# Kernel tuning notes

Measured on AMD Instinct MI355X. Metric: run time of the kernel, lower is better.

Reference implementation:

```python
import jax, jax.numpy as jnp
import numpy as np

B, C_IN, IMG = 4, 1, 256
E, P = 800, 4            # embed_size, patch_size
H, DH, M = 8, 64, 64     # heads, dim_head=heads**2, num_landmarks
N = (IMG // P) ** 2      # 4096 tokens
OUT = 256                # output_size
RESK = 33                # lucidrains residual depthwise conv kernel
BN_EPS = 1e-5
LN_EPS = 1e-5
PINV_ITERS = 6


def setup_inputs() -> dict:
    key = jax.random.key(0)
    ks = iter(jax.random.split(key, 32))
    def nrm(shape, s=0.02):
        return jax.random.normal(next(ks), shape, jnp.float32) * s
    inp = {"x": jax.random.normal(next(ks), (B, C_IN, IMG, IMG), jnp.float32)}
    # conv stack: (in, out, kernel); last conv has stride=P, padding=0
    for i, (ci, co, kk) in enumerate([(C_IN, 64, 3), (64, 128, 3), (128, 256, 3), (256, E, P)]):
        inp[f"w{i}"] = nrm((co, ci, kk, kk), 0.05)
        inp[f"b{i}"] = jnp.zeros((co,), jnp.float32)
        inp[f"g{i}"] = jnp.ones((co,), jnp.float32)    # BN gamma
        inp[f"be{i}"] = jnp.zeros((co,), jnp.float32)  # BN beta
        inp[f"mu{i}"] = nrm((co,), 0.1)                # BN running mean
        inp[f"var{i}"] = jax.random.uniform(next(ks), (co,), jnp.float32, 0.5, 1.5)
    inp["qkv_w"] = nrm((E, 3 * H * DH))      # to_qkv (no bias)
    inp["out_w"] = nrm((H * DH, E))          # to_out linear
    inp["out_b"] = jnp.zeros((E,), jnp.float32)
    inp["res_w"] = nrm((H, 1, RESK, 1), 0.05)  # depthwise residual conv over token dim
    inp["ln_g"] = jnp.ones((E,), jnp.float32)
    inp["ln_b"] = jnp.zeros((E,), jnp.float32)
    inp["head_w"] = nrm((E, OUT * OUT // N))   # Linear(800, 16)
    inp["head_b"] = jnp.zeros((OUT * OUT // N,), jnp.float32)
    return inp


def conv2d(x, w, b, stride, pad):
    y = jax.lax.conv_general_dilated(x, w, (stride, stride), [(pad, pad), (pad, pad)],
                                     dimension_numbers=("NCHW", "OIHW", "NCHW"))
    return y + b[None, :, None, None]


def bn(x, g, be, mu, var):
    s = g * jax.lax.rsqrt(var + BN_EPS)  # eval-mode BatchNorm
    return x * s[None, :, None, None] + (be - mu * s)[None, :, None, None]


def moore_penrose_pinv(a, iters=PINV_ITERS):
    I = jnp.eye(a.shape[-1], dtype=a.dtype)
    z = jnp.swapaxes(a, -1, -2) / (jnp.max(jnp.abs(a).sum(-1)) * jnp.max(jnp.abs(a).sum(-2)))
    for _ in range(iters):
        az = a @ z
        z = 0.25 * z @ (13.0 * I - az @ (15.0 * I - az @ (7.0 * I - az)))
    return z


def reference(x, w0, b0, g0, be0, mu0, var0, w1, b1, g1, be1, mu1, var1,
              w2, b2, g2, be2, mu2, var2, w3, b3, g3, be3, mu3, var3,
              qkv_w, out_w, out_b, res_w, ln_g, ln_b, head_w, head_b):
    # ---- PatchEmbedConv ----
    h = x
    blocks = [(w0, b0, g0, be0, mu0, var0, 1, 1), (w1, b1, g1, be1, mu1, var1, 1, 1),
              (w2, b2, g2, be2, mu2, var2, 1, 1), (w3, b3, g3, be3, mu3, var3, P, 0)]
    for w, b, g, be, mu, var, st, pd in blocks:
        h = jax.nn.relu(bn(conv2d(h, w, b, st, pd), g, be, mu, var))
    tok = h.reshape(B, E, N).transpose(0, 2, 1)  # [B, N, E]

    # ---- NystromAttention (n % m == 0, so no front padding needed) ----
    qkv = tok @ qkv_w  # [B, N, 3*H*DH]
    q, k, v = [t.reshape(B, N, H, DH).transpose(0, 2, 1, 3) for t in jnp.split(qkv, 3, axis=-1)]
    q = q * (DH ** -0.5)
    l = N // M
    q_l = q.reshape(B, H, M, l, DH).mean(3)  # landmark means over consecutive blocks
    k_l = k.reshape(B, H, M, l, DH).mean(3)
    a1 = jax.nn.softmax(jnp.einsum("bhnd,bhmd->bhnm", q, k_l), axis=-1)    # [B,H,N,M]
    a2 = jax.nn.softmax(jnp.einsum("bhmd,bhkd->bhmk", q_l, k_l), axis=-1)  # [B,H,M,M]
    a3 = jax.nn.softmax(jnp.einsum("bhmd,bhnd->bhmn", q_l, k), axis=-1)    # [B,H,M,N]
    out = (a1 @ moore_penrose_pinv(a2)) @ (a3 @ v)  # [B,H,N,DH]
    # residual depthwise conv over the token dim of v (groups = heads)
    res = jax.lax.conv_general_dilated(v, res_w, (1, 1), [(RESK // 2, RESK // 2), (0, 0)],
                                       dimension_numbers=("NCHW", "OIHW", "NCHW"),
                                       feature_group_count=H)
    out = out + res
    out = out.transpose(0, 2, 1, 3).reshape(B, N, H * DH)
    out = out @ out_w + out_b  # [B, N, E]

    # ---- LayerNorm ----
    mu_t = out.mean(-1, keepdims=True)
    var_t = out.var(-1, keepdims=True)
    out = (out - mu_t) * jax.lax.rsqrt(var_t + LN_EPS) * ln_g + ln_b

    # ---- reconstruction head ----
    y = jax.nn.sigmoid(out @ head_w + head_b)  # [B, N, OUT*OUT/N]
    return y.reshape(-1, 1, OUT, OUT)
```

## Files before the change

### kernel.cpp

```cpp
#include <hip/hip_runtime.h>

#define DI __device__ __forceinline__

constexpr float BN_EPS_C = 1e-5f;
constexpr float LN_EPS_C = 1e-5f;

typedef _Float16 half8 __attribute__((ext_vector_type(8)));
typedef float f32x4 __attribute__((ext_vector_type(4)));

constexpr size_t B_H0   = 0;
constexpr size_t B_H1   = 8388608;
constexpr size_t B_H2   = 25165824;
constexpr size_t B_Q    = 25165824;
constexpr size_t B_V    = 58720256;
constexpr size_t B_KT   = 75497472;
constexpr size_t B_ATT  = 92274688;
constexpr size_t B_LNB  = 25165824;
constexpr size_t B_TOK  = 159383552;
constexpr size_t B_WP1  = 185597952;
constexpr size_t B_WP2  = 185745408;
constexpr size_t B_WP3  = 186335232;
constexpr size_t B_QKVT = 192888832;
constexpr size_t B_OWT  = 195346432;
constexpr size_t B_QL   = 196165632;
constexpr size_t B_KL   = 196689920;
constexpr size_t B_KLH  = 197214208;
constexpr size_t B_A2   = 197476352;
constexpr size_t B_W2T  = 198524928;
constexpr size_t B_A3V  = 198787072;
constexpr size_t B_SCAL = 199311360;
constexpr size_t B_HWH  = 199311424;

DI void gl_lds16(const _Float16* g, _Float16* l) {
  __builtin_amdgcn_global_load_lds(
      (const __attribute__((address_space(1))) void*)g,
      (__attribute__((address_space(3))) void*)l, 16, 0, 0);
}

template <int LP, int RP>
DI void mm16v(const float* L, const float* R, int r0, int c0, float reg[4][4]) {
  #pragma unroll
  for (int i = 0; i < 4; ++i)
    #pragma unroll
    for (int j = 0; j < 4; ++j) reg[i][j] = 0.f;
  #pragma unroll 4
  for (int dd = 0; dd < 64; dd += 4) {
    f32x4 l[4], rv[4];
    #pragma unroll
    for (int i = 0; i < 4; ++i)
      l[i] = *reinterpret_cast<const f32x4*>(&L[(size_t)(r0 + i) * LP + dd]);
    #pragma unroll
    for (int u = 0; u < 4; ++u)
      rv[u] = *reinterpret_cast<const f32x4*>(&R[(size_t)(dd + u) * RP + c0]);
    #pragma unroll
    for (int i = 0; i < 4; ++i)
      #pragma unroll
      for (int u = 0; u < 4; ++u)
        #pragma unroll
        for (int j = 0; j < 4; ++j)
          reg[i][j] = fmaf(l[i][u], rv[u][j], reg[i][j]);
  }
}

__global__ void k_pack_all(
    const float* __restrict__ w1, const float* __restrict__ w2c, const float* __restrict__ w3,
    const float* __restrict__ qkvw, const float* __restrict__ outw, const float* __restrict__ headw,
    _Float16* __restrict__ wp1, _Float16* __restrict__ wp2, _Float16* __restrict__ wp3,
    _Float16* __restrict__ qkvT, _Float16* __restrict__ owT, _Float16* __restrict__ hwh,
    float* __restrict__ scal) {
  size_t i = (size_t)blockIdx.x * 256 + threadIdx.x;
  if (i < 73728) {
    int q = i % 9, ci = (i / 9) % 64, co = i / (9 * 64);
    wp1[((size_t)co * 9 + q) * 64 + ci] = (_Float16)w1[i];
  } else if (i < 368640) {
    size_t j = i - 73728;
    int q = j % 9, ci = (j / 9) % 128, co = j / (9 * 128);
    wp2[((size_t)co * 9 + q) * 128 + ci] = (_Float16)w2c[j];
  } else if (i < 3645440) {
    size_t j = i - 368640;
    int q = j % 16, ci = (j / 16) % 256, co = j / (16 * 256);
    wp3[((size_t)co * 16 + q) * 256 + ci] = (_Float16)w3[j];
  } else if (i < 4874240) {
    size_t j = i - 3645440;
    int n = j % 1536, k = j / 1536;
    qkvT[(size_t)n * 800 + k] = (_Float16)qkvw[j];
  } else if (i < 5283840) {
    size_t j = i - 4874240;
    int n = j % 800, k = j / 800;
    owT[(size_t)n * 512 + k] = (_Float16)outw[j];
  } else if (i < 5296640) {
    size_t j = i - 5283840;
    int n = j % 16, k = j / 16;
    hwh[(size_t)n * 800 + k] = (_Float16)headw[j];
  } else if (i < 5296642) {
    scal[i - 5296640] = 0.f;
  }
}

__global__ __launch_bounds__(256) void k_conv0(
    const float* __restrict__ xb, const float* __restrict__ w0, const float* __restrict__ b0,
    const float* __restrict__ g0, const float* __restrict__ be0, const float* __restrict__ mu0,
    const float* __restrict__ var0, _Float16* __restrict__ h0) {
  const int t = threadIdx.x, co = t & 63, xg = t >> 6;
  const int y = blockIdx.x;
  const int x0 = blockIdx.y * 64 + xg * 16;
  float wreg[9];
  #pragma unroll
  for (int q = 0; q < 9; ++q) wreg[q] = w0[co * 9 + q];
  float s = g0[co] * rsqrtf(var0[co] + BN_EPS_C);
  float sh = fmaf(b0[co] - mu0[co], s, be0[co]);
  #pragma unroll 4
  for (int xl = 0; xl < 16; ++xl) {
    int xx = x0 + xl;
    float acc = 0.f;
    #pragma unroll
    for (int dy = 0; dy < 3; ++dy) {
      int yy = y + dy - 1;
      if ((unsigned)yy >= 256u) continue;
      #pragma unroll
      for (int dx = 0; dx < 3; ++dx) {
        int xi = xx + dx - 1;
        if ((unsigned)xi >= 256u) continue;
        acc = fmaf(wreg[dy * 3 + dx], xb[yy * 256 + xi], acc);
      }
    }
    float v = fmaxf(fmaf(acc, s, sh), 0.f);
    h0[((size_t)y * 256 + xx) * 64 + co] = (_Float16)v;
  }
}

template <int CI>
__global__ __launch_bounds__(256) void k_convs(
    const _Float16* __restrict__ in, const _Float16* __restrict__ wp,
    const float* __restrict__ bias, const float* __restrict__ g, const float* __restrict__ be,
    const float* __restrict__ mu, const float* __restrict__ var,
    _Float16* __restrict__ out, int CO, int NCT) {
  __shared__ _Float16 Ab[2][128 * 40];
  __shared__ _Float16 Bb[2][128 * 40];
  constexpr int CPQ = CI / 32;
  constexpr int NCK = 9 * CPQ;
  const int t = threadIdx.x;
  const int bid = blockIdx.x;
  const int xcd = bid & 7, slot = bid >> 3;
  const int pj = slot / NCT, cc = slot % NCT;
  const int p = pj * 8 + xcd;
  const int r0 = p * 128, c0 = cc * 128;

  const int ma = t >> 2, kga = t & 3;
  int ry[2], rx[2];
  #pragma unroll
  for (int s = 0; s < 2; ++s) {
    int r = r0 + ma + s * 64;
    ry[s] = r >> 8;
    rx[s] = r & 255;
  }
  const _Float16* baseB[2];
  #pragma unroll
  for (int s = 0; s < 2; ++s)
    baseB[s] = wp + (size_t)(c0 + ma + s * 64) * 9 * CI + kga * 8;
  const int wo = ma * 40 + kga * 8;

  auto loadA = [&](int s, int ck) -> half8 {
    int q = ck / CPQ, coff = (ck % CPQ) * 32;
    int yy = ry[s] + q / 3 - 1;
    int xx = rx[s] + q % 3 - 1;
    half8 a = {};
    if ((unsigned)yy < 256u && (unsigned)xx < 256u)
      a = *reinterpret_cast<const half8*>(in + ((size_t)yy * 256 + xx) * CI + coff + kga * 8);
    return a;
  };

  {
    half8 a0 = loadA(0, 0), a1 = loadA(1, 0);
    half8 b0v = *reinterpret_cast<const half8*>(baseB[0]);
    half8 b1v = *reinterpret_cast<const half8*>(baseB[1]);
    *reinterpret_cast<half8*>(&Ab[0][wo]) = a0;
    *reinterpret_cast<half8*>(&Ab[0][wo + 2560]) = a1;
    *reinterpret_cast<half8*>(&Bb[0][wo]) = b0v;
    *reinterpret_cast<half8*>(&Bb[0][wo + 2560]) = b1v;
  }
  __syncthreads();

  const int w = t >> 6, lo = t & 15, hi = (t >> 4) & 3;
  const int wm = w >> 1, wn = w & 1;
  const int roA = (wm * 64 + lo) * 40 + 8 * hi;
  const int roB = (wn * 64 + lo) * 40 + 8 * hi;
  f32x4 acc[4][4] = {};

  for (int ck = 0; ck < NCK; ++ck) {
    const int cur = ck & 1;
    const bool more = (ck + 1 < NCK);
    half8 rA0, rA1, rB0, rB1;
    if (more) {
      rA0 = loadA(0, ck + 1);
      rA1 = loadA(1, ck + 1);
      rB0 = *reinterpret_cast<const half8*>(baseB[0] + (ck + 1) * 32);
      rB1 = *reinterpret_cast<const half8*>(baseB[1] + (ck + 1) * 32);
    }
    half8 af[4], bf[4];
    #pragma unroll
    for (int mi = 0; mi < 4; ++mi)
      af[mi] = *reinterpret_cast<const half8*>(&Ab[cur][roA + mi * 640]);
    #pragma unroll
    for (int ni = 0; ni < 4; ++ni)
      bf[ni] = *reinterpret_cast<const half8*>(&Bb[cur][roB + ni * 640]);
    #pragma unroll
    for (int mi = 0; mi < 4; ++mi)
      #pragma unroll
      for (int ni = 0; ni < 4; ++ni)
        acc[mi][ni] = __builtin_amdgcn_mfma_f32_16x16x32_f16(af[mi], bf[ni], acc[mi][ni], 0, 0, 0);
    if (more) {
      *reinterpret_cast<half8*>(&Ab[cur ^ 1][wo]) = rA0;
      *reinterpret_cast<half8*>(&Ab[cur ^ 1][wo + 2560]) = rA1;
      *reinterpret_cast<half8*>(&Bb[cur ^ 1][wo]) = rB0;
      *reinterpret_cast<half8*>(&Bb[cur ^ 1][wo + 2560]) = rB1;
    }
    __syncthreads();
  }

  #pragma unroll
  for (int ni = 0; ni < 4; ++ni) {
    int co = c0 + wn * 64 + ni * 16 + lo;
    float s = g[co] * rsqrtf(var[co] + BN_EPS_C);
    float sh = fmaf(bias[co] - mu[co], s, be[co]);
    #pragma unroll
    for (int mi = 0; mi < 4; ++mi)
      #pragma unroll
      for (int rr = 0; rr < 4; ++rr) {
        int row = r0 + wm * 64 + mi * 16 + hi * 4 + rr;
        float v = fmaxf(fmaf(acc[mi][ni][rr], s, sh), 0.f);
        out[(size_t)row * CO + co] = (_Float16)v;
      }
  }
}

__global__ __launch_bounds__(256) void k_c3(
    const _Float16* __restrict__ h2, const _Float16* __restrict__ wp3,
    const float* __restrict__ b3, const float* __restrict__ g3, const float* __restrict__ be3,
    const float* __restrict__ mu3, const float* __restrict__ var3,
    _Float16* __restrict__ tok) {
  __shared__ _Float16 Abuf[2][128 * 32];
  __shared__ _Float16 Bbuf[2][160 * 32];
  const int t = threadIdx.x;
  const int bid = blockIdx.x;
  const int xcd = bid & 7, slot = bid >> 3;
  const int pj = slot / 5, cc = slot % 5;
  const int p = pj * 8 + xcd;
  const int r0 = p * 128, c0 = cc * 160;
  const int img = r0 >> 12;
  const _Float16* h2i = h2 + (size_t)img * 16777216;

  const int w = t >> 6, l = t & 63;
  const int kslot = (l & 3) ^ ((l >> 3) & 3);
  const _Float16* gA[2];
  #pragma unroll
  for (int s = 0; s < 2; ++s) {
    int mar = 16 * w + (l >> 2) + 64 * s;
    int r = r0 + mar;
    int py = (r & 4095) >> 6, px = r & 63;
    gA[s] = h2i + ((size_t)py * 1024 + px * 4) * 256 + kslot * 8;
  }
  const _Float16* gB[3];
  #pragma unroll
  for (int s = 0; s < 3; ++s) {
    int rb = 16 * w + (l >> 2) + 64 * s;
    if (rb > 159) rb = 159;
    gB[s] = wp3 + (size_t)(c0 + rb) * 4096 + kslot * 8;
  }

  const int lo = t & 15, hi = (t >> 4) & 3;
  const int wm = w >> 1, wn = w & 1;
  const int sl = hi ^ ((lo >> 1) & 3);
  const int roA = (wm * 64 + lo) * 32 + sl * 8;
  const int roB = (wn * 80 + lo) * 32 + sl * 8;

  f32x4 acc[4][5] = {};

  auto STAGE = [&](int buf, int ck) {
    const int kn = ck << 5;
    const int q = kn >> 8;
    const size_t aoff = (size_t)(q >> 2) * 65536 + (size_t)(q & 3) * 256 + (kn & 255);
    _Float16* Ad = &Abuf[buf][512 * w];
    _Float16* Bd = &Bbuf[buf][512 * w];
    gl_lds16(gA[0] + aoff, Ad);
    gl_lds16(gA[1] + aoff, Ad + 2048);
    gl_lds16(gB[0] + kn, Bd);
    gl_lds16(gB[1] + kn, Bd + 2048);
    if (w < 2) gl_lds16(gB[2] + kn, Bd + 4096);
  };

  STAGE(0, 0);
  __syncthreads();

  for (int ck = 0; ck < 128; ++ck) {
    const int cur = ck & 1;
    if (ck + 1 < 128) STAGE(cur ^ 1, ck + 1);
    half8 af[4], bf[5];
    #pragma unroll
    for (int mi = 0; mi < 4; ++mi)
      af[mi] = *reinterpret_cast<const half8*>(&Abuf[cur][roA + mi * 512]);
    #pragma unroll
    for (int ni = 0; ni < 5; ++ni)
      bf[ni] = *reinterpret_cast<const half8*>(&Bbuf[cur][roB + ni * 512]);
    #pragma unroll
    for (int mi = 0; mi < 4; ++mi)
      #pragma unroll
      for (int ni = 0; ni < 5; ++ni)
        acc[mi][ni] = __builtin_amdgcn_mfma_f32_16x16x32_f16(af[mi], bf[ni], acc[mi][ni], 0, 0, 0);
    __syncthreads();
  }

  #pragma unroll
  for (int ni = 0; ni < 5; ++ni) {
    int col = c0 + wn * 80 + ni * 16 + lo;
    float s = g3[col] * rsqrtf(var3[col] + BN_EPS_C);
    float sh = fmaf(b3[col] - mu3[col], s, be3[col]);
    #pragma unroll
    for (int mi = 0; mi < 4; ++mi)
      #pragma unroll
      for (int rr = 0; rr < 4; ++rr) {
        int row = r0 + wm * 64 + mi * 16 + hi * 4 + rr;
        float v = fmaxf(fmaf(acc[mi][ni][rr], s, sh), 0.f);
        tok[(size_t)row * 800 + col] = (_Float16)v;
      }
  }
}

__global__ __launch_bounds__(256) void k_qkv_s(
    const _Float16* __restrict__ tok, const _Float16* __restrict__ qkvT,
    _Float16* __restrict__ qx, _Float16* __restrict__ kTg, _Float16* __restrict__ vx,
    float* __restrict__ ql, float* __restrict__ kl, _Float16* __restrict__ klh) {
  __shared__ _Float16 SH[20480];
  _Float16* AbP = SH;
  _Float16* BbP = SH + 10240;
  const int t = threadIdx.x;
  const int bid = blockIdx.x;
  const int xcd = bid & 7, slot = bid >> 3;
  const int pj = slot / 12, cc = slot % 12;
  const int p = pj * 8 + xcd;
  const int r0 = p * 128, c0 = cc * 128;

  const int ma = t >> 2, kga = t & 3;
  const _Float16* baseA[2];
  const _Float16* baseB[2];
  #pragma unroll
  for (int s = 0; s < 2; ++s) {
    baseA[s] = tok + (size_t)(r0 + ma + s * 64) * 800 + kga * 8;
    baseB[s] = qkvT + (size_t)(c0 + ma + s * 64) * 800 + kga * 8;
  }
  const int wo = ma * 40 + kga * 8;

  {
    half8 a0 = *reinterpret_cast<const half8*>(baseA[0]);
    half8 a1 = *reinterpret_cast<const half8*>(baseA[1]);
    half8 b0v = *reinterpret_cast<const half8*>(baseB[0]);
    half8 b1v = *reinterpret_cast<const half8*>(baseB[1]);
    *reinterpret_cast<half8*>(&AbP[wo]) = a0;
    *reinterpret_cast<half8*>(&AbP[wo + 2560]) = a1;
    *reinterpret_cast<half8*>(&BbP[wo]) = b0v;
    *reinterpret_cast<half8*>(&BbP[wo + 2560]) = b1v;
  }
  __syncthreads();

  const int w = t >> 6, lo = t & 15, hi = (t >> 4) & 3;
  const int wm = w >> 1, wn = w & 1;
  const int roA = (wm * 64 + lo) * 40 + 8 * hi;
  const int roB = (wn * 64 + lo) * 40 + 8 * hi;
  f32x4 acc[4][4] = {};

  for (int ck = 0; ck < 25; ++ck) {
    const int cur = ck & 1;
    const bool more = (ck + 1 < 25);
    half8 rA0, rA1, rB0, rB1;
    if (more) {
      const int kn = (ck + 1) * 32;
      rA0 = *reinterpret_cast<const half8*>(baseA[0] + kn);
      rA1 = *reinterpret_cast<const half8*>(baseA[1] + kn);
      rB0 = *reinterpret_cast<const half8*>(baseB[0] + kn);
      rB1 = *reinterpret_cast<const half8*>(baseB[1] + kn);
    }
    half8 af[4], bf[4];
    #pragma unroll
    for (int mi = 0; mi < 4; ++mi)
      af[mi] = *reinterpret_cast<const half8*>(&AbP[cur * 5120 + roA + mi * 640]);
    #pragma unroll
    for (int ni = 0; ni < 4; ++ni)
      bf[ni] = *reinterpret_cast<const half8*>(&BbP[cur * 5120 + roB + ni * 640]);
    #pragma unroll
    for (int mi = 0; mi < 4; ++mi)
      #pragma unroll
      for (int ni = 0; ni < 4; ++ni)
        acc[mi][ni] = __builtin_amdgcn_mfma_f32_16x16x32_f16(af[mi], bf[ni], acc[mi][ni], 0, 0, 0);
    if (more) {
      *reinterpret_cast<half8*>(&AbP[(cur ^ 1) * 5120 + wo]) = rA0;
      *reinterpret_cast<half8*>(&AbP[(cur ^ 1) * 5120 + wo + 2560]) = rA1;
      *reinterpret_cast<half8*>(&BbP[(cur ^ 1) * 5120 + wo]) = rB0;
      *reinterpret_cast<half8*>(&BbP[(cur ^ 1) * 5120 + wo + 2560]) = rB1;
    }
    __syncthreads();
  }

  const int seg = cc >> 2;
  const int b = r0 >> 12;
  const int m = ((r0 & 4095) >> 6) + wm;
  if (seg == 1) {
    #pragma unroll
    for (int ni = 0; ni < 4; ++ni) {
      int cl = wn * 64 + ni * 16 + lo;
      #pragma unroll
      for (int mi = 0; mi < 4; ++mi)
        #pragma unroll
        for (int rr = 0; rr < 4; ++rr) {
          int nl = wm * 64 + mi * 16 + hi * 4 + rr;
          SH[cl * 136 + nl] = (_Float16)acc[mi][ni][rr];
        }
    }
    __syncthreads();
    const int base_row = b * 512 + (cc & 3) * 128;
    const int base_n = (p & 31) * 128;
    #pragma unroll
    for (int e = t; e < 2048; e += 256) {
      int cl = e >> 4, ch = e & 15;
      half8 vvv = *reinterpret_cast<const half8*>(&SH[cl * 136 + ch * 8]);
      *reinterpret_cast<half8*>(&kTg[(size_t)(base_row + cl) * 4096 + base_n + ch * 8]) = vvv;
    }
  } else {
    const float scale = (seg == 0) ? 0.125f : 1.0f;
    _Float16* dst = (seg == 0) ? qx : vx;
    #pragma unroll
    for (int ni = 0; ni < 4; ++ni) {
      int cseg = (cc & 3) * 128 + wn * 64 + ni * 16 + lo;
      int h = cseg >> 6, d = cseg & 63;
      #pragma unroll
      for (int mi = 0; mi < 4; ++mi)
        #pragma unroll
        for (int rr = 0; rr < 4; ++rr) {
          int row = r0 + wm * 64 + mi * 16 + hi * 4 + rr;
          int nn = row & 4095;
          dst[((size_t)(b * 8 + h) * 4096 + nn) * 64 + d] = (_Float16)(acc[mi][ni][rr] * scale);
        }
    }
  }
  if (seg <= 1) {
    const float lscale = ((seg == 0) ? 0.125f : 1.0f) * (1.f / 64.f);
    #pragma unroll
    for (int ni = 0; ni < 4; ++ni) {
      float sum = 0.f;
      #pragma unroll
      for (int mi = 0; mi < 4; ++mi)
        #pragma unroll
        for (int rr = 0; rr < 4; ++rr) sum += acc[mi][ni][rr];
      sum += __shfl_xor(sum, 16);
      sum += __shfl_xor(sum, 32);
      if (hi == 0) {
        int cseg = (cc & 3) * 128 + wn * 64 + ni * 16 + lo;
        int h = cseg >> 6, d = cseg & 63;
        int bh = b * 8 + h;
        float lm = sum * lscale;
        if (seg == 0) {
          ql[((size_t)bh * 64 + m) * 64 + d] = lm;
        } else {
          kl[((size_t)bh * 64 + m) * 64 + d] = lm;
          klh[((size_t)bh * 64 + m) * 64 + d] = (_Float16)lm;
        }
      }
    }
  }
}

__global__ __launch_bounds__(256) void k_op_s(
    const _Float16* __restrict__ attb, const _Float16* __restrict__ owT,
    const float* __restrict__ ob, _Float16* __restrict__ lnb) {
  __shared__ _Float16 Abuf[2][128 * 40];
  __shared__ _Float16 Bbuf[2][160 * 40];
  const int t = threadIdx.x;
  const int bid = blockIdx.x;
  const int xcd = bid & 7, slot = bid >> 3;
  const int pj = slot / 5, cc = slot % 5;
  const int p = pj * 8 + xcd;
  const int r0 = p * 128, c0 = cc * 160;

  const int ma = t >> 2, kga = t & 3;
  const _Float16* baseA[2];
  #pragma unroll
  for (int s = 0; s < 2; ++s)
    baseA[s] = attb + (size_t)(r0 + ma + s * 64) * 512 + kga * 8;
  const _Float16* baseB[3];
  #pragma unroll
  for (int s = 0; s < 3; ++s) {
    int cb = ma + s * 64;
    baseB[s] = owT + (size_t)(c0 + (cb < 160 ? cb : 159)) * 512 + kga * 8;
  }
  const int wo = ma * 40 + kga * 8;

  const int w = t >> 6, lo = t & 15, hi = (t >> 4) & 3;
  const int wm = w >> 1, wn = w & 1;
  const int roA = (wm * 64 + lo) * 40 + 8 * hi;
  const int roB = (wn * 80 + lo) * 40 + 8 * hi;

  f32x4 acc[4][5] = {};

  {
    half8 a0 = *reinterpret_cast<const half8*>(baseA[0]);
    half8 a1 = *reinterpret_cast<const half8*>(baseA[1]);
    half8 b0v = *reinterpret_cast<const half8*>(baseB[0]);
    half8 b1v = *reinterpret_cast<const half8*>(baseB[1]);
    *reinterpret_cast<half8*>(&Abuf[0][wo]) = a0;
    *reinterpret_cast<half8*>(&Abuf[0][wo + 2560]) = a1;
    *reinterpret_cast<half8*>(&Bbuf[0][wo]) = b0v;
    *reinterpret_cast<half8*>(&Bbuf[0][wo + 2560]) = b1v;
    if (t < 128) {
      half8 b2v = *reinterpret_cast<const half8*>(baseB[2]);
      *reinterpret_cast<half8*>(&Bbuf[0][wo + 5120]) = b2v;
    }
  }
  __syncthreads();

  for (int ck = 0; ck < 16; ++ck) {
    const int cur = ck & 1;
    const bool more = (ck + 1 < 16);
    half8 rA0, rA1, rB0, rB1, rB2;
    if (more) {
      const int kn = (ck + 1) << 5;
      rA0 = *reinterpret_cast<const half8*>(baseA[0] + kn);
      rA1 = *reinterpret_cast<const half8*>(baseA[1] + kn);
      rB0 = *reinterpret_cast<const half8*>(baseB[0] + kn);
      rB1 = *reinterpret_cast<const half8*>(baseB[1] + kn);
      if (t < 128) rB2 = *reinterpret_cast<const half8*>(baseB[2] + kn);
    }
    half8 af[4], bf[5];
    #pragma unroll
    for (int mi = 0; mi < 4; ++mi)
      af[mi] = *reinterpret_cast<const half8*>(&Abuf[cur][roA + mi * 640]);
    #pragma unroll
    for (int ni = 0; ni < 5; ++ni)
      bf[ni] = *reinterpret_cast<const half8*>(&Bbuf[cur][roB + ni * 640]);
    #pragma unroll
    for (int mi = 0; mi < 4; ++mi)
      #pragma unroll
      for (int ni = 0; ni < 5; ++ni)
        acc[mi][ni] = __builtin_amdgcn_mfma_f32_16x16x32_f16(af[mi], bf[ni], acc[mi][ni], 0, 0, 0);
    if (more) {
      *reinterpret_cast<half8*>(&Abuf[cur ^ 1][wo]) = rA0;
      *reinterpret_cast<half8*>(&Abuf[cur ^ 1][wo + 2560]) = rA1;
      *reinterpret_cast<half8*>(&Bbuf[cur ^ 1][wo]) = rB0;
      *reinterpret_cast<half8*>(&Bbuf[cur ^ 1][wo + 2560]) = rB1;
      if (t < 128) *reinterpret_cast<half8*>(&Bbuf[cur ^ 1][wo + 5120]) = rB2;
    }
    __syncthreads();
  }

  #pragma unroll
  for (int ni = 0; ni < 5; ++ni) {
    int col = c0 + wn * 80 + ni * 16 + lo;
    float bv = ob[col];
    #pragma unroll
    for (int mi = 0; mi < 4; ++mi)
      #pragma unroll
      for (int rr = 0; rr < 4; ++rr) {
        int row = r0 + wm * 64 + mi * 16 + hi * 4 + rr;
        lnb[(size_t)row * 800 + col] = (_Float16)(acc[mi][ni][rr] + bv);
      }
  }
}

__global__ __launch_bounds__(64) void k_a2(
    const float* __restrict__ ql, const float* __restrict__ kl,
    float* __restrict__ a2, float* __restrict__ scal) {
  __shared__ float sp[64 * 65];
  const int bh = blockIdx.x, t = threadIdx.x;
  const float* qr = ql + ((size_t)bh * 64 + t) * 64;
  const float* kb = kl + (size_t)bh * 4096;
  float mx = -1e30f;
  for (int c = 0; c < 64; ++c) {
    float acc = 0.f;
    #pragma unroll 8
    for (int dd = 0; dd < 64; ++dd) acc = fmaf(qr[dd], kb[c * 64 + dd], acc);
    sp[t * 65 + c] = acc;
    mx = fmaxf(mx, acc);
  }
  float sum = 0.f;
  for (int c = 0; c < 64; ++c) {
    float e = expf(sp[t * 65 + c] - mx);
    sp[t * 65 + c] = e;
    sum += e;
  }
  float inv = 1.f / sum;
  float rs = 0.f;
  for (int c = 0; c < 64; ++c) {
    float p = sp[t * 65 + c] * inv;
    sp[t * 65 + c] = p;
    a2[(size_t)bh * 4096 + t * 64 + c] = p;
    rs += p;
  }
  atomicMax(reinterpret_cast<int*>(scal), __float_as_int(rs));
  __syncthreads();
  float cs = 0.f;
  for (int r = 0; r < 64; ++r) cs += sp[r * 65 + t];
  atomicMax(reinterpret_cast<int*>(scal) + 1, __float_as_int(cs));
}

__global__ __launch_bounds__(256) void k_a3v(
    const float* __restrict__ ql, const _Float16* __restrict__ kT,
    const _Float16* __restrict__ vx, float* __restrict__ a3v) {
  __shared__ float sq[64];
  __shared__ float sP[4096];
  __shared__ float red[4];
  __shared__ float red2[4][64];
  const int t = threadIdx.x;
  const int m = blockIdx.x, bh = blockIdx.y;
  if (t < 64) sq[t] = ql[((size_t)bh * 64 + m) * 64 + t];
  __syncthreads();
  const _Float16* kb = kT + (size_t)bh * 262144;
  float sc[16];
  #pragma unroll
  for (int i = 0; i < 16; ++i) sc[i] = 0.f;
  for (int dd = 0; dd < 64; ++dd) {
    float qv = sq[dd];
    const half8* kr = reinterpret_cast<const half8*>(kb + (size_t)dd * 4096 + t * 16);
    half8 k0 = kr[0], k1 = kr[1];
    #pragma unroll
    for (int i = 0; i < 8; ++i) sc[i] = fmaf(qv, (float)k0[i], sc[i]);
    #pragma unroll
    for (int i = 0; i < 8; ++i) sc[8 + i] = fmaf(qv, (float)k1[i], sc[8 + i]);
  }
  float mx = sc[0];
  #pragma unroll
  for (int i = 1; i < 16; ++i) mx = fmaxf(mx, sc[i]);
  #pragma unroll
  for (int o = 32; o; o >>= 1) mx = fmaxf(mx, __shfl_xor(mx, o));
  if ((t & 63) == 0) red[t >> 6] = mx;
  __syncthreads();
  mx = fmaxf(fmaxf(red[0], red[1]), fmaxf(red[2], red[3]));
  __syncthreads();
  float sum = 0.f;
  #pragma unroll
  for (int i = 0; i < 16; ++i) {
    sc[i] = expf(sc[i] - mx);
    sum += sc[i];
  }
  #pragma unroll
  for (int o = 32; o; o >>= 1) sum += __shfl_xor(sum, o);
  if ((t & 63) == 0) red[t >> 6] = sum;
  __syncthreads();
  sum = red[0] + red[1] + red[2] + red[3];
  float inv = 1.f / sum;
  #pragma unroll
  for (int i = 0; i < 16; ++i) sP[t * 16 + i] = sc[i] * inv;
  __syncthreads();
  const int seg = t >> 6, l = t & 63;
  const int nl = l >> 3, dblk = (l & 7) * 8;
  const _Float16* vb = vx + (size_t)bh * 262144;
  float acc8[8] = {};
  for (int it = 0; it < 128; ++it) {
    int n8 = seg * 1024 + it * 8;
    half8 vv = *reinterpret_cast<const half8*>(&vb[(size_t)(n8 + nl) * 64 + dblk]);
    float pc = sP[n8 + nl];
    #pragma unroll
    for (int u = 0; u < 8; ++u) acc8[u] = fmaf(pc, (float)vv[u], acc8[u]);
  }
  #pragma unroll
  for (int off = 8; off <= 32; off <<= 1)
    #pragma unroll
    for (int u = 0; u < 8; ++u) acc8[u] += __shfl_xor(acc8[u], off);
  if (nl == 0) {
    #pragma unroll
    for (int u = 0; u < 8; ++u) red2[seg][dblk + u] = acc8[u];
  }
  __syncthreads();
  if (seg == 0)
    a3v[((size_t)bh * 64 + m) * 64 + l] = red2[0][l] + red2[1][l] + red2[2][l] + red2[3][l];
}

__global__ __launch_bounds__(256) void k_pinv(
    const float* __restrict__ a2g, const float* __restrict__ scal,
    const float* __restrict__ a3vg, _Float16* __restrict__ w2t) {
  __shared__ float z[64 * 68];
  __shared__ float az[64 * 68];
  __shared__ float tb[64 * 68];
  const int bh = blockIdx.x, t = threadIdx.x;
  const int r0 = (t >> 4) << 2, c0 = (t & 15) << 2;
  const float* ag = a2g + (size_t)bh * 4096;
  const float denom = 1.f / (scal[0] * scal[1]);
  #pragma unroll
  for (int i = 0; i < 4; ++i)
    #pragma unroll
    for (int j = 0; j < 4; ++j)
      z[(r0 + i) * 68 + c0 + j] = ag[(c0 + j) * 64 + r0 + i] * denom;
  __syncthreads();
  float reg[4][4], val[4][4];
  for (int it = 0; it < 6; ++it) {
    mm16v<64, 68>(ag, z, r0, c0, reg);
    #pragma unroll
    for (int i = 0; i < 4; ++i)
      #pragma unroll
      for (int j = 0; j < 4; ++j) az[(r0 + i) * 68 + c0 + j] = reg[i][j];
    __syncthreads();
    mm16v<68, 68>(az, az, r0, c0, reg);
    #pragma unroll
    for (int i = 0; i < 4; ++i)
      #pragma unroll
      for (int j = 0; j < 4; ++j)
        tb[(r0 + i) * 68 + c0 + j] = 7.f * az[(r0 + i) * 68 + c0 + j] - reg[i][j];
    __syncthreads();
    mm16v<68, 68>(az, tb, r0, c0, reg);
    #pragma unroll
    for (int i = 0; i < 4; ++i)
      #pragma unroll
      for (int j = 0; j < 4; ++j)
        val[i][j] = 15.f * az[(r0 + i) * 68 + c0 + j] - reg[i][j];
    __syncthreads();
    #pragma unroll
    for (int i = 0; i < 4; ++i)
      #pragma unroll
      for (int j = 0; j < 4; ++j) tb[(r0 + i) * 68 + c0 + j] = val[i][j];
    __syncthreads();
    mm16v<68, 68>(z, tb, r0, c0, reg);
    #pragma unroll
    for (int i = 0; i < 4; ++i)
      #pragma unroll
      for (int j = 0; j < 4; ++j)
        val[i][j] = 0.25f * (13.f * z[(r0 + i) * 68 + c0 + j] - reg[i][j]);
    __syncthreads();
    #pragma unroll
    for (int i = 0; i < 4; ++i)
      #pragma unroll
      for (int j = 0; j < 4; ++j) z[(r0 + i) * 68 + c0 + j] = val[i][j];
    __syncthreads();
  }
  mm16v<68, 64>(z, a3vg + (size_t)bh * 4096, r0, c0, reg);
  #pragma unroll
  for (int i = 0; i < 4; ++i)
    #pragma unroll
    for (int j = 0; j < 4; ++j)
      w2t[(size_t)bh * 4096 + (c0 + j) * 64 + (r0 + i)] = (_Float16)reg[i][j];
}

__global__ __launch_bounds__(256) void k_combine_m(
    const _Float16* __restrict__ qx, const _Float16* __restrict__ klh,
    const _Float16* __restrict__ w2t, const _Float16* __restrict__ vx,
    const float* __restrict__ rw, _Float16* __restrict__ att) {
  __shared__ _Float16 sP[64 * 72];
  __shared__ _Float16 sVT[64 * 104];
  __shared__ _Float16 sT[64 * 104];
  __shared__ float sR[33];
  const int t = threadIdx.x, w = t >> 6, lo = t & 15, hi = (t >> 4) & 3;
  const int n0 = blockIdx.x * 64;
  const int h = blockIdx.y, b = blockIdx.z, bh = b * 8 + h;
  if (t < 33) sR[t] = rw[h * 33 + t];
  __syncthreads();
  const _Float16* vb = vx + (size_t)bh * 262144;
  #pragma unroll
  for (int u = 0; u < 24; ++u) {
    int e = t + u * 256;
    int r = e >> 6, d = e & 63;
    int nn = n0 - 16 + r;
    sVT[d * 104 + r] = ((unsigned)nn < 4096u) ? vb[(size_t)nn * 64 + d] : (_Float16)0.f;
  }
  #pragma unroll
  for (int u = 0; u < 24; ++u) {
    int e = t + u * 256;
    int r = e % 96, i = e / 96;
    int j = r - i;
    sT[i * 104 + r] = (j >= 0 && j < 33) ? (_Float16)sR[j] : (_Float16)0.f;
  }
  f32x4 sa[4] = {};
  const _Float16* qp = qx + ((size_t)bh * 4096 + n0 + w * 16 + lo) * 64 + 8 * hi;
  const _Float16* klp = klh + (size_t)bh * 4096;
  #pragma unroll
  for (int c = 0; c < 2; ++c) {
    half8 a = *reinterpret_cast<const half8*>(qp + 32 * c);
    #pragma unroll
    for (int ct = 0; ct < 4; ++ct) {
      half8 bf = *reinterpret_cast<const half8*>(klp + (size_t)(ct * 16 + lo) * 64 + 8 * hi + 32 * c);
      sa[ct] = __builtin_amdgcn_mfma_f32_16x16x32_f16(a, bf, sa[ct], 0, 0, 0);
    }
  }
  #pragma unroll
  for (int r = 0; r < 4; ++r) {
    float mx = fmaxf(fmaxf(sa[0][r], sa[1][r]), fmaxf(sa[2][r], sa[3][r]));
    #pragma unroll
    for (int o = 8; o; o >>= 1) mx = fmaxf(mx, __shfl_xor(mx, o));
    float e0 = expf(sa[0][r] - mx), e1 = expf(sa[1][r] - mx);
    float e2 = expf(sa[2][r] - mx), e3 = expf(sa[3][r] - mx);
    float sm = e0 + e1 + e2 + e3;
    #pragma unroll
    for (int o = 8; o; o >>= 1) sm += __shfl_xor(sm, o);
    float inv = 1.f / sm;
    int row = w * 16 + hi * 4 + r;
    sP[row * 72 + lo] = (_Float16)(e0 * inv);
    sP[row * 72 + 16 + lo] = (_Float16)(e1 * inv);
    sP[row * 72 + 32 + lo] = (_Float16)(e2 * inv);
    sP[row * 72 + 48 + lo] = (_Float16)(e3 * inv);
  }
  __syncthreads();
  f32x4 ao[4] = {};
  const _Float16* w2p = w2t + (size_t)bh * 4096;
  #pragma unroll
  for (int c = 0; c < 2; ++c) {
    half8 a = *reinterpret_cast<const half8*>(&sP[(w * 16 + lo) * 72 + 8 * hi + 32 * c]);
    #pragma unroll
    for (int ct = 0; ct < 4; ++ct) {
      half8 bf = *reinterpret_cast<const half8*>(w2p + (size_t)(ct * 16 + lo) * 64 + 8 * hi + 32 * c);
      ao[ct] = __builtin_amdgcn_mfma_f32_16x16x32_f16(a, bf, ao[ct], 0, 0, 0);
    }
  }
  #pragma unroll
  for (int c = 0; c < 3; ++c) {
    half8 a = *reinterpret_cast<const half8*>(&sT[(w * 16 + lo) * 104 + 8 * hi + 32 * c]);
    #pragma unroll
    for (int ct = 0; ct < 4; ++ct) {
      half8 bf = *reinterpret_cast<const half8*>(&sVT[(ct * 16 + lo) * 104 + 8 * hi + 32 * c]);
      ao[ct] = __builtin_amdgcn_mfma_f32_16x16x32_f16(a, bf, ao[ct], 0, 0, 0);
    }
  }
  _Float16* ab = att + ((size_t)b * 4096) * 512 + (size_t)h * 64;
  #pragma unroll
  for (int ct = 0; ct < 4; ++ct)
    #pragma unroll
    for (int r = 0; r < 4; ++r) {
      int n = n0 + w * 16 + hi * 4 + r;
      ab[(size_t)n * 512 + ct * 16 + lo] = (_Float16)ao[ct][r];
    }
}

__global__ __launch_bounds__(256) void k_lnhead(
    const _Float16* __restrict__ ln, const _Float16* __restrict__ hwh,
    const float* __restrict__ g, const float* __restrict__ bb,
    const float* __restrict__ hb, float* __restrict__ out) {
  const int t = threadIdx.x, w = t >> 6, lo = t & 15, hi = (t >> 4) & 3;
  const int row0 = blockIdx.x * 64 + w * 16;
  const _Float16* ap = ln + (size_t)(row0 + lo) * 800 + 8 * hi;
  float s1 = 0.f, s2 = 0.f;
  #pragma unroll 5
  for (int k = 0; k < 800; k += 32) {
    half8 a = *reinterpret_cast<const half8*>(ap + k);
    #pragma unroll
    for (int u = 0; u < 8; ++u) {
      float x = (float)a[u];
      s1 += x;
      s2 = fmaf(x, x, s2);
    }
  }
  s1 += __shfl_xor(s1, 16); s1 += __shfl_xor(s1, 32);
  s2 += __shfl_xor(s2, 16); s2 += __shfl_xor(s2, 32);
  float mean = s1 * (1.f / 800.f);
  float var = s2 * (1.f / 800.f) - mean * mean;
  float rstd = rsqrtf(var + LN_EPS_C);
  const _Float16* bp = hwh + (size_t)lo * 800 + 8 * hi;
  f32x4 acc = {};
  #pragma unroll 5
  for (int k = 0; k < 800; k += 32) {
    half8 a = *reinterpret_cast<const half8*>(ap + k);
    half8 an;
    #pragma unroll
    for (int u = 0; u < 8; ++u) {
      int kk = k + 8 * hi + u;
      float x = ((float)a[u] - mean) * rstd * g[kk] + bb[kk];
      an[u] = (_Float16)x;
    }
    half8 b = *reinterpret_cast<const half8*>(bp + k);
    acc = __builtin_amdgcn_mfma_f32_16x16x32_f16(an, b, acc, 0, 0, 0);
  }
  float bv = hb[lo];
  #pragma unroll
  for (int r = 0; r < 4; ++r) {
    int row = row0 + hi * 4 + r;
    out[(size_t)row * 16 + lo] = 1.f / (1.f + expf(-(acc[r] + bv)));
  }
}

extern "C" void kernel_launch(void* const* d_in, const int* in_sizes, int n_in,
                              void* d_out, int out_size, void* d_ws, size_t ws_size,
                              hipStream_t stream) {
  (void)in_sizes; (void)n_in; (void)out_size; (void)ws_size;
  const float* x     = (const float*)d_in[0];
  const float* w0    = (const float*)d_in[1];
  const float* b0    = (const float*)d_in[2];
  const float* g0    = (const float*)d_in[3];
  const float* be0   = (const float*)d_in[4];
  const float* mu0   = (const float*)d_in[5];
  const float* var0  = (const float*)d_in[6];
  const float* w1    = (const float*)d_in[7];
  const float* b1    = (const float*)d_in[8];
  const float* g1    = (const float*)d_in[9];
  const float* be1   = (const float*)d_in[10];
  const float* mu1   = (const float*)d_in[11];
  const float* var1  = (const float*)d_in[12];
  const float* w2c   = (const float*)d_in[13];
  const float* b2    = (const float*)d_in[14];
  const float* g2    = (const float*)d_in[15];
  const float* be2   = (const float*)d_in[16];
  const float* mu2   = (const float*)d_in[17];
  const float* var2  = (const float*)d_in[18];
  const float* w3    = (const float*)d_in[19];
  const float* b3    = (const float*)d_in[20];
  const float* g3    = (const float*)d_in[21];
  const float* be3   = (const float*)d_in[22];
  const float* mu3   = (const float*)d_in[23];
  const float* var3  = (const float*)d_in[24];
  const float* qkvw  = (const float*)d_in[25];
  const float* outw  = (const float*)d_in[26];
  const float* outbv = (const float*)d_in[27];
  const float* resw  = (const float*)d_in[28];
  const float* lng   = (const float*)d_in[29];
  const float* lnbv  = (const float*)d_in[30];
  const float* headw = (const float*)d_in[31];
  const float* headb = (const float*)d_in[32];

  char* wsb = (char*)d_ws;
  _Float16* h0   = (_Float16*)(wsb + B_H0);
  _Float16* h1   = (_Float16*)(wsb + B_H1);
  _Float16* h2   = (_Float16*)(wsb + B_H2);
  _Float16* qb   = (_Float16*)(wsb + B_Q);
  _Float16* vb   = (_Float16*)(wsb + B_V);
  _Float16* kT   = (_Float16*)(wsb + B_KT);
  _Float16* tok  = (_Float16*)(wsb + B_TOK);
  _Float16* attb = (_Float16*)(wsb + B_ATT);
  _Float16* wp1  = (_Float16*)(wsb + B_WP1);
  _Float16* wp2  = (_Float16*)(wsb + B_WP2);
  _Float16* wp3  = (_Float16*)(wsb + B_WP3);
  _Float16* qkvT = (_Float16*)(wsb + B_QKVT);
  _Float16* owT  = (_Float16*)(wsb + B_OWT);
  _Float16* klh  = (_Float16*)(wsb + B_KLH);
  _Float16* w2t  = (_Float16*)(wsb + B_W2T);
  _Float16* hwh  = (_Float16*)(wsb + B_HWH);
  _Float16* lnb16 = (_Float16*)(wsb + B_LNB);
  float* ql   = (float*)(wsb + B_QL);
  float* kl   = (float*)(wsb + B_KL);
  float* a2   = (float*)(wsb + B_A2);
  float* a3v  = (float*)(wsb + B_A3V);
  float* scal = (float*)(wsb + B_SCAL);

  k_pack_all<<<dim3(20691), 256, 0, stream>>>(
      w1, w2c, w3, qkvw, outw, headw, wp1, wp2, wp3, qkvT, owT, hwh, scal);

  for (int img = 0; img < 4; ++img) {
    k_conv0<<<dim3(256, 4), 256, 0, stream>>>(
        x + (size_t)img * 65536, w0, b0, g0, be0, mu0, var0, h0);
    k_convs<64><<<dim3(512), 256, 0, stream>>>(
        h0, wp1, b1, g1, be1, mu1, var1, h1, 128, 1);
    k_convs<128><<<dim3(1024), 256, 0, stream>>>(
        h1, wp2, b2, g2, be2, mu2, var2, h2 + (size_t)img * 16777216, 256, 2);
  }
  k_c3<<<dim3(640), 256, 0, stream>>>(h2, wp3, b3, g3, be3, mu3, var3, tok);
  k_qkv_s<<<dim3(1536), 256, 0, stream>>>(tok, qkvT, qb, kT, vb, ql, kl, klh);
  k_a2<<<dim3(32), 64, 0, stream>>>(ql, kl, a2, scal);
  k_a3v<<<dim3(64, 32), 256, 0, stream>>>(ql, kT, vb, a3v);
  k_pinv<<<dim3(32), 256, 0, stream>>>(a2, scal, a3v, w2t);
  k_combine_m<<<dim3(64, 8, 4), 256, 0, stream>>>(qb, klh, w2t, vb, resw, attb);
  k_op_s<<<dim3(640), 256, 0, stream>>>(attb, owT, outbv, lnb16);
  k_lnhead<<<dim3(256), 256, 0, stream>>>(lnb16, hwh, lng, lnbv, headb, (float*)d_out);
}
```

Before: 940.3 us.

## Stage GEMM tiles with direct global-to-LDS loads and XOR-swizzled layout

Three MFMA GEMM kernels (the 3x3 convs, the QKV projection and the output projection) now stage their operand tiles with global_load_lds straight into shared memory, replacing the register round trip. The padded 40-element row stride is replaced by an unpadded 32-element stride with an XOR swizzle to avoid bank conflicts. Out-of-bounds conv taps read from a small zeroed global page, since the direct-to-LDS path cannot insert zeros. The aim is to cut VGPR pressure and LDS write instructions and to shrink the shared-memory footprint, at the cost of relying on the swizzle mapping and load ordering being correct.

Result: no change. 938.3 us (-0.2%).

```diff
diff --git a/kernel.cpp b/kernel.cpp
--- a/kernel.cpp
+++ b/kernel.cpp
@@ -30,6 +30,7 @@
 constexpr size_t B_A3V  = 198787072;
 constexpr size_t B_SCAL = 199311360;
 constexpr size_t B_HWH  = 199311424;
+constexpr size_t B_ZPG  = 199337024;
 
 DI void gl_lds16(const _Float16* g, _Float16* l) {
   __builtin_amdgcn_global_load_lds(
@@ -67,7 +68,7 @@
     const float* __restrict__ qkvw, const float* __restrict__ outw, const float* __restrict__ headw,
     _Float16* __restrict__ wp1, _Float16* __restrict__ wp2, _Float16* __restrict__ wp3,
     _Float16* __restrict__ qkvT, _Float16* __restrict__ owT, _Float16* __restrict__ hwh,
-    float* __restrict__ scal) {
+    float* __restrict__ scal, float* __restrict__ zpg) {
   size_t i = (size_t)blockIdx.x * 256 + threadIdx.x;
   if (i < 73728) {
     int q = i % 9, ci = (i / 9) % 64, co = i / (9 * 64);
@@ -94,6 +95,8 @@
     hwh[(size_t)n * 800 + k] = (_Float16)headw[j];
   } else if (i < 5296642) {
     scal[i - 5296640] = 0.f;
+  } else if (i < 5296650) {
+    zpg[i - 5296642] = 0.f;
   }
 }
 
@@ -134,9 +137,9 @@
     const _Float16* __restrict__ in, const _Float16* __restrict__ wp,
     const float* __restrict__ bias, const float* __restrict__ g, const float* __restrict__ be,
     const float* __restrict__ mu, const float* __restrict__ var,
-    _Float16* __restrict__ out, int CO, int NCT) {
-  __shared__ _Float16 Ab[2][128 * 40];
-  __shared__ _Float16 Bb[2][128 * 40];
+    _Float16* __restrict__ out, int CO, int NCT, const _Float16* __restrict__ zpg) {
+  __shared__ _Float16 Ab[2][128 * 32];
+  __shared__ _Float16 Bb[2][128 * 32];
   constexpr int CPQ = CI / 32;
   constexpr int NCK = 9 * CPQ;
   const int t = threadIdx.x;
@@ -146,75 +149,63 @@
   const int p = pj * 8 + xcd;
   const int r0 = p * 128, c0 = cc * 128;
 
-  const int ma = t >> 2, kga = t & 3;
+  const int w = t >> 6, l = t & 63;
+  const int kslot = (l & 3) ^ ((l >> 3) & 3);
   int ry[2], rx[2];
   #pragma unroll
   for (int s = 0; s < 2; ++s) {
-    int r = r0 + ma + s * 64;
+    int r = r0 + 16 * w + (l >> 2) + 64 * s;
     ry[s] = r >> 8;
     rx[s] = r & 255;
   }
-  const _Float16* baseB[2];
+  const _Float16* gB[2];
   #pragma unroll
   for (int s = 0; s < 2; ++s)
-    baseB[s] = wp + (size_t)(c0 + ma + s * 64) * 9 * CI + kga * 8;
-  const int wo = ma * 40 + kga * 8;
-
-  auto loadA = [&](int s, int ck) -> half8 {
-    int q = ck / CPQ, coff = (ck % CPQ) * 32;
-    int yy = ry[s] + q / 3 - 1;
-    int xx = rx[s] + q % 3 - 1;
-    half8 a = {};
-    if ((unsigned)yy < 256u && (unsigned)xx < 256u)
-      a = *reinterpret_cast<const half8*>(in + ((size_t)yy * 256 + xx) * CI + coff + kga * 8);
-    return a;
+    gB[s] = wp + (size_t)(c0 + 16 * w + (l >> 2) + 64 * s) * 9 * CI + kslot * 8;
+
+  const int lo = t & 15, hi = (t >> 4) & 3;
+  const int wm = w >> 1, wn = w & 1;
+  const int sl = hi ^ ((lo >> 1) & 3);
+  const int roA = (wm * 64 + lo) * 32 + sl * 8;
+  const int roB = (wn * 64 + lo) * 32 + sl * 8;
+  f32x4 acc[4][4] = {};
+
+  auto STAGE = [&](int buf, int ck) {
+    const int q = ck / CPQ, coff = (ck % CPQ) * 32;
+    const int dy = q / 3 - 1, dx = q % 3 - 1;
+    _Float16* Ad = &Ab[buf][512 * w];
+    _Float16* Bd = &Bb[buf][512 * w];
+    #pragma unroll
+    for (int s = 0; s < 2; ++s) {
+      int yy = ry[s] + dy, xx = rx[s] + dx;
+      const _Float16* src =
+          ((unsigned)yy < 256u && (unsigned)xx < 256u)
+              ? in + ((size_t)yy * 256 + xx) * CI + coff + kslot * 8
+              : zpg;
+      gl_lds16(src, Ad + s * 2048);
+    }
+    gl_lds16(gB[0] + ck * 32, Bd);
+    gl_lds16(gB[1] + ck * 32, Bd + 2048);
   };
 
-  {
-    half8 a0 = loadA(0, 0), a1 = loadA(1, 0);
-    half8 b0v = *reinterpret_cast<const half8*>(baseB[0]);
-    half8 b1v = *reinterpret_cast<const half8*>(baseB[1]);
-    *reinterpret_cast<half8*>(&Ab[0][wo]) = a0;
-    *reinterpret_cast<half8*>(&Ab[0][wo + 2560]) = a1;
-    *reinterpret_cast<half8*>(&Bb[0][wo]) = b0v;
-    *reinterpret_cast<half8*>(&Bb[0][wo + 2560]) = b1v;
-  }
-  __syncthreads();
-
-  const int w = t >> 6, lo = t & 15, hi = (t >> 4) & 3;
-  const int wm = w >> 1, wn = w & 1;
-  const int roA = (wm * 64 + lo) * 40 + 8 * hi;
-  const int roB = (wn * 64 + lo) * 40 + 8 * hi;
-  f32x4 acc[4][4] = {};
+  STAGE(0, 0);
+  __syncthreads();
 
   for (int ck = 0; ck < NCK; ++ck) {
     const int cur = ck & 1;
-    const bool more = (ck + 1 < NCK);
-    half8 rA0, rA1, rB0, rB1;
-    if (more) {
-      rA0 = loadA(0, ck + 1);
-      rA1 = loadA(1, ck + 1);
-      rB0 = *reinterpret_cast<const half8*>(baseB[0] + (ck + 1) * 32);
-      rB1 = *reinterpret_cast<const half8*>(baseB[1] + (ck + 1) * 32);
-    }
+    if (ck + 1 < NCK) STAGE(cur ^ 1, ck + 1);
     half8 af[4], bf[4];
     #pragma unroll
     for (int mi = 0; mi < 4; ++mi)
-      af[mi] = *reinterpret_cast<const half8*>(&Ab[cur][roA + mi * 640]);
+      af[mi] = *reinterpret_cast<const half8*>(&Ab[cur][roA + mi * 512]);
     #pragma unroll
     for (int ni = 0; ni < 4; ++ni)
-      bf[ni] = *reinterpret_cast<const half8*>(&Bb[cur][roB + ni * 640]);
+      bf[ni] = *reinterpret_cast<const half8*>(&Bb[cur][roB + ni * 512]);
     #pragma unroll
     for (int mi = 0; mi < 4; ++mi)
       #pragma unroll
       for (int ni = 0; ni < 4; ++ni)
         acc[mi][ni] = __builtin_amdgcn_mfma_f32_16x16x32_f16(af[mi], bf[ni], acc[mi][ni], 0, 0, 0);
-    if (more) {
-      *reinterpret_cast<half8*>(&Ab[cur ^ 1][wo]) = rA0;
-      *reinterpret_cast<half8*>(&Ab[cur ^ 1][wo + 2560]) = rA1;
-      *reinterpret_cast<half8*>(&Bb[cur ^ 1][wo]) = rB0;
-      *reinterpret_cast<half8*>(&Bb[cur ^ 1][wo + 2560]) = rB1;
-    }
     __syncthreads();
   }
 
@@ -330,9 +321,9 @@
     const _Float16* __restrict__ tok, const _Float16* __restrict__ qkvT,
     _Float16* __restrict__ qx, _Float16* __restrict__ kTg, _Float16* __restrict__ vx,
     float* __restrict__ ql, float* __restrict__ kl, _Float16* __restrict__ klh) {
-  __shared__ _Float16 SH[20480];
+  __shared__ _Float16 SH[17408];
   _Float16* AbP = SH;
-  _Float16* BbP = SH + 10240;
+  _Float16* BbP = SH + 8192;
   const int t = threadIdx.x;
   const int bid = blockIdx.x;
   const int xcd = bid & 7, slot = bid >> 3;
@@ -340,63 +331,52 @@
   const int p = pj * 8 + xcd;
   const int r0 = p * 128, c0 = cc * 128;
 
-  const int ma = t >> 2, kga = t & 3;
-  const _Float16* baseA[2];
-  const _Float16* baseB[2];
+  const int w = t >> 6, l = t & 63;
+  const int kslot = (l & 3) ^ ((l >> 3) & 3);
+  const _Float16* gA[2];
+  const _Float16* gB[2];
   #pragma unroll
   for (int s = 0; s < 2; ++s) {
-    baseA[s] = tok + (size_t)(r0 + ma + s * 64) * 800 + kga * 8;
-    baseB[s] = qkvT + (size_t)(c0 + ma + s * 64) * 800 + kga * 8;
-  }
-  const int wo = ma * 40 + kga * 8;
-
-  {
-    half8 a0 = *reinterpret_cast<const half8*>(baseA[0]);
-    half8 a1 = *reinterpret_cast<const half8*>(baseA[1]);
-    half8 b0v = *reinterpret_cast<const half8*>(baseB[0]);
-    half8 b1v = *reinterpret_cast<const half8*>(baseB[1]);
-    *reinterpret_cast<half8*>(&AbP[wo]) = a0;
-    *reinterpret_cast<half8*>(&AbP[wo + 2560]) = a1;
-    *reinterpret_cast<half8*>(&BbP[wo]) = b0v;
-    *reinterpret_cast<half8*>(&BbP[wo + 2560]) = b1v;
-  }
-  __syncthreads();
-
-  const int w = t >> 6, lo = t & 15, hi = (t >> 4) & 3;
+    int mar = 16 * w + (l >> 2) + 64 * s;
+    gA[s] = tok + (size_t)(r0 + mar) * 800 + kslot * 8;
+    gB[s] = qkvT + (size_t)(c0 + mar) * 800 + kslot * 8;
+  }
+
+  const int lo = t & 15, hi = (t >> 4) & 3;
   const int wm = w >> 1, wn = w & 1;
-  const int roA = (wm * 64 + lo) * 40 + 8 * hi;
-  const int roB = (wn * 64 + lo) * 40 + 8 * hi;
+  const int sl = hi ^ ((lo >> 1) & 3);
+  const int roA = (wm * 64 + lo) * 32 + sl * 8;
+  const int roB = (wn * 64 + lo) * 32 + sl * 8;
   f32x4 acc[4][4] = {};
+
+  auto STAGE = [&](int buf, int ck) {
+    const int kn = ck * 32;
+    _Float16* Ad = &AbP[buf * 4096 + 512 * w];
+    _Float16* Bd = &BbP[buf * 4096 + 512 * w];
+    gl_lds16(gA[0] + kn, Ad);
+    gl_lds16(gA[1] + kn, Ad + 2048);
+    gl_lds16(gB[0] + kn, Bd);
+    gl_lds16(gB[1] + kn, Bd + 2048);
+  };
+
+  STAGE(0, 0);
+  __syncthreads();
 
   for (int ck = 0; ck < 25; ++ck) {
     const int cur = ck & 1;
-    const bool more = (ck + 1 < 25);
-    half8 rA0, rA1, rB0, rB1;
-    if (more) {
-      const int kn = (ck + 1) * 32;
-      rA0 = *reinterpret_cast<const half8*>(baseA[0] + kn);
-      rA1 = *reinterpret_cast<const half8*>(baseA[1] + kn);
-      rB0 = *reinterpret_cast<const half8*>(baseB[0] + kn);
-      rB1 = *reinterpret_cast<const half8*>(baseB[1] + kn);
-    }
+    if (ck + 1 < 25) STAGE(cur ^ 1, ck + 1);
     half8 af[4], bf[4];
     #pragma unroll
     for (int mi = 0; mi < 4; ++mi)
-      af[mi] = *reinterpret_cast<const half8*>(&AbP[cur * 5120 + roA + mi * 640]);
+      af[mi] = *reinterpret_cast<const half8*>(&AbP[cur * 4096 + roA + mi * 512]);
     #pragma unroll
     for (int ni = 0; ni < 4; ++ni)
-      bf[ni] = *reinterpret_cast<const half8*>(&BbP[cur * 5120 + roB + ni * 640]);
+      bf[ni] = *reinterpret_cast<const half8*>(&BbP[cur * 4096 + roB + ni * 512]);
     #pragma unroll
     for (int mi = 0; mi < 4; ++mi)
       #pragma unroll
       for (int ni = 0; ni < 4; ++ni)
         acc[mi][ni] = __builtin_amdgcn_mfma_f32_16x16x32_f16(af[mi], bf[ni], acc[mi][ni], 0, 0, 0);
-    if (more) {
-      *reinterpret_cast<half8*>(&AbP[(cur ^ 1) * 5120 + wo]) = rA0;
-      *reinterpret_cast<half8*>(&AbP[(cur ^ 1) * 5120 + wo + 2560]) = rA1;
-      *reinterpret_cast<half8*>(&BbP[(cur ^ 1) * 5120 + wo]) = rB0;
-      *reinterpret_cast<half8*>(&BbP[(cur ^ 1) * 5120 + wo + 2560]) = rB1;
-    }
     __syncthreads();
   }
 
@@ -471,8 +451,8 @@
 __global__ __launch_bounds__(256) void k_op_s(
     const _Float16* __restrict__ attb, const _Float16* __restrict__ owT,
     const float* __restrict__ ob, _Float16* __restrict__ lnb) {
-  __shared__ _Float16 Abuf[2][128 * 40];
-  __shared__ _Float16 Bbuf[2][160 * 40];
+  __shared__ _Float16 Abuf[2][128 * 32];
+  __shared__ _Float16 Bbuf[2][160 * 32];
   const int t = threadIdx.x;
   const int bid = blockIdx.x;
   const int xcd = bid & 7, slot = bid >> 3;
@@ -480,73 +460,59 @@
   const int p = pj * 8 + xcd;
   const int r0 = p * 128, c0 = cc * 160;
 
-  const int ma = t >> 2, kga = t & 3;
-  const _Float16* baseA[2];
-  #pragma unroll
-  for (int s = 0; s < 2; ++s)
-    baseA[s] = attb + (size_t)(r0 + ma + s * 64) * 512 + kga * 8;
-  const _Float16* baseB[3];
+  const int w = t >> 6, l = t & 63;
+  const int kslot = (l & 3) ^ ((l >> 3) & 3);
+  const _Float16* gA[2];
+  #pragma unroll
+  for (int s = 0; s < 2; ++s) {
+    int mar = 16 * w + (l >> 2) + 64 * s;
+    gA[s] = attb + (size_t)(r0 + mar) * 512 + kslot * 8;
+  }
+  const _Float16* gB[3];
   #pragma unroll
   for (int s = 0; s < 3; ++s) {
-    int cb = ma + s * 64;
-    baseB[s] = owT + (size_t)(c0 + (cb < 160 ? cb : 159)) * 512 + kga * 8;
-  }
-  const int wo = ma * 40 + kga * 8;
-
-  const int w = t >> 6, lo = t & 15, hi = (t >> 4) & 3;
+    int rb = 16 * w + (l >> 2) + 64 * s;
+    if (rb > 159) rb = 159;
+    gB[s] = owT + (size_t)(c0 + rb) * 512 + kslot * 8;
+  }
+
+  const int lo = t & 15, hi = (t >> 4) & 3;
   const int wm = w >> 1, wn = w & 1;
-  const int roA = (wm * 64 + lo) * 40 + 8 * hi;
-  const int roB = (wn * 80 + lo) * 40 + 8 * hi;
+  const int sl = hi ^ ((lo >> 1) & 3);
+  const int roA = (wm * 64 + lo) * 32 + sl * 8;
+  const int roB = (wn * 80 + lo) * 32 + sl * 8;
 
   f32x4 acc[4][5] = {};
 
-  {
-    half8 a0 = *reinterpret_cast<const half8*>(baseA[0]);
-    half8 a1 = *reinterpret_cast<const half8*>(baseA[1]);
-    half8 b0v = *reinterpret_cast<const half8*>(baseB[0]);
-    half8 b1v = *reinterpret_cast<const half8*>(baseB[1]);
-    *reinterpret_cast<half8*>(&Abuf[0][wo]) = a0;
-    *reinterpret_cast<half8*>(&Abuf[0][wo + 2560]) = a1;
-    *reinterpret_cast<half8*>(&Bbuf[0][wo]) = b0v;
-    *reinterpret_cast<half8*>(&Bbuf[0][wo + 2560]) = b1v;
-    if (t < 128) {
-      half8 b2v = *reinterpret_cast<const half8*>(baseB[2]);
-      *reinterpret_cast<half8*>(&Bbuf[0][wo + 5120]) = b2v;
-    }
-  }
+  auto STAGE = [&](int buf, int ck) {
+    const int kn = ck << 5;
+    _Float16* Ad = &Abuf[buf][512 * w];
+    _Float16* Bd = &Bbuf[buf][512 * w];
+    gl_lds16(gA[0] + kn, Ad);
+    gl_lds16(gA[1] + kn, Ad + 2048);
+    gl_lds16(gB[0] + kn, Bd);
+    gl_lds16(gB[1] + kn, Bd + 2048);
+    if (w < 2) gl_lds16(gB[2] + kn, Bd + 4096);
+  };
+
+  STAGE(0, 0);
   __syncthreads();
 
   for (int ck = 0; ck < 16; ++ck) {
     const int cur = ck & 1;
-    const bool more = (ck + 1 < 16);
-    half8 rA0, rA1, rB0, rB1, rB2;
-    if (more) {
-      const int kn = (ck + 1) << 5;
-      rA0 = *reinterpret_cast<const half8*>(baseA[0] + kn);
-      rA1 = *reinterpret_cast<const half8*>(baseA[1] + kn);
-      rB0 = *reinterpret_cast<const half8*>(baseB[0] + kn);
-      rB1 = *reinterpret_cast<const half8*>(baseB[1] + kn);
-      if (t < 128) rB2 = *reinterpret_cast<const half8*>(baseB[2] + kn);
-    }
+    if (ck + 1 < 16) STAGE(cur ^ 1, ck + 1);
     half8 af[4], bf[5];
     #pragma unroll
     for (int mi = 0; mi < 4; ++mi)
-      af[mi] = *reinterpret_cast<const half8*>(&Abuf[cur][roA + mi * 640]);
+      af[mi] = *reinterpret_cast<const half8*>(&Abuf[cur][roA + mi * 512]);
     #pragma unroll
     for (int ni = 0; ni < 5; ++ni)
-      bf[ni] = *reinterpret_cast<const half8*>(&Bbuf[cur][roB + ni * 640]);
+      bf[ni] = *reinterpret_cast<const half8*>(&Bbuf[cur][roB + ni * 512]);
     #pragma unroll
     for (int mi = 0; mi < 4; ++mi)
       #pragma unroll
       for (int ni = 0; ni < 5; ++ni)
         acc[mi][ni] = __builtin_amdgcn_mfma_f32_16x16x32_f16(af[mi], bf[ni], acc[mi][ni], 0, 0, 0);
-    if (more) {
-      *reinterpret_cast<half8*>(&Abuf[cur ^ 1][wo]) = rA0;
-      *reinterpret_cast<half8*>(&Abuf[cur ^ 1][wo + 2560]) = rA1;
-      *reinterpret_cast<half8*>(&Bbuf[cur ^ 1][wo]) = rB0;
-      *reinterpret_cast<half8*>(&Bbuf[cur ^ 1][wo + 2560]) = rB1;
-      if (t < 128) *reinterpret_cast<half8*>(&Bbuf[cur ^ 1][wo + 5120]) = rB2;
-    }
     __syncthreads();
   }
 
@@ -926,6 +892,7 @@
   _Float16* w2t  = (_Float16*)(wsb + B_W2T);
   _Float16* hwh  = (_Float16*)(wsb + B_HWH);
   _Float16* lnb16 = (_Float16*)(wsb + B_LNB);
+  _Float16* zpg  = (_Float16*)(wsb + B_ZPG);
   float* ql   = (float*)(wsb + B_QL);
   float* kl   = (float*)(wsb + B_KL);
   float* a2   = (float*)(wsb + B_A2);
@@ -933,15 +900,15 @@
   float* scal = (float*)(wsb + B_SCAL);
 
   k_pack_all<<<dim3(20691), 256, 0, stream>>>(
-      w1, w2c, w3, qkvw, outw, headw, wp1, wp2, wp3, qkvT, owT, hwh, scal);
+      w1, w2c, w3, qkvw, outw, headw, wp1, wp2, wp3, qkvT, owT, hwh, scal, (float*)zpg);
 
   for (int img = 0; img < 4; ++img) {
     k_conv0<<<dim3(256, 4), 256, 0, stream>>>(
         x + (size_t)img * 65536, w0, b0, g0, be0, mu0, var0, h0);
     k_convs<64><<<dim3(512), 256, 0, stream>>>(
-        h0, wp1, b1, g1, be1, mu1, var1, h1, 128, 1);
+        h0, wp1, b1, g1, be1, mu1, var1, h1, 128, 1, zpg);
     k_convs<128><<<dim3(1024), 256, 0, stream>>>(
-        h1, wp2, b2, g2, be2, mu2, var2, h2 + (size_t)img * 16777216, 256, 2);
+        h1, wp2, b2, g2, be2, mu2, var2, h2 + (size_t)img * 16777216, 256, 2, zpg);
   }
   k_c3<<<dim3(640), 256, 0, stream>>>(h2, wp3, b3, g3, be3, mu3, var3, tok);
   k_qkv_s<<<dim3(1536), 256, 0, stream>>>(tok, qkvT, qb, kT, vb, ql, kl, klh);
```
